# Optimization experiments

Hardware: AMD Instinct MI355X
Metric: run time of the kernel (lower is better)

The kernel has to match this reference:

```python
import math
import jax, jax.numpy as jnp
import numpy as np

B, T, C = 4, 2048, 1024
NH, HD = 16, C // 16
FF = 4096
EPS = 1e-5


def _layernorm(x, g, b):
    mu = jnp.mean(x, axis=-1, keepdims=True)
    var = jnp.mean(jnp.square(x - mu), axis=-1, keepdims=True)
    return (x - mu) * jax.lax.rsqrt(var + EPS) * g + b


def _new_gelu(x):
    c = math.sqrt(2.0 / math.pi)
    return 0.5 * x * (1.0 + jnp.tanh(c * (x + 0.044715 * x * x * x)))


def setup_inputs() -> dict:
    key = jax.random.key(0)
    ks = jax.random.split(key, 5)
    s = lambda fan_in: 1.0 / math.sqrt(fan_in)
    return {
        "x": jax.random.normal(ks[0], (B, T, C), jnp.float32),
        "ln1_g": jnp.ones((C,), jnp.float32),
        "ln1_b": jnp.zeros((C,), jnp.float32),
        "w_qkv": jax.random.normal(ks[1], (C, 3 * C), jnp.float32) * s(C),
        "b_qkv": jnp.zeros((3 * C,), jnp.float32),
        "w_attn_proj": jax.random.normal(ks[2], (C, C), jnp.float32) * s(C),
        "b_attn_proj": jnp.zeros((C,), jnp.float32),
        "ln2_g": jnp.ones((C,), jnp.float32),
        "ln2_b": jnp.zeros((C,), jnp.float32),
        "w_fc": jax.random.normal(ks[3], (C, FF), jnp.float32) * s(C),
        "b_fc": jnp.zeros((FF,), jnp.float32),
        "w_mlp_proj": jax.random.normal(ks[4], (FF, C), jnp.float32) * s(FF),
        "b_mlp_proj": jnp.zeros((C,), jnp.float32),
    }


def reference(x, ln1_g, ln1_b, w_qkv, b_qkv, w_attn_proj, b_attn_proj,
              ln2_g, ln2_b, w_fc, b_fc, w_mlp_proj, b_mlp_proj):
    # --- attention branch ---
    h = _layernorm(x, ln1_g, ln1_b)
    qkv = h @ w_qkv + b_qkv                      # [B,T,3C]
    q, k, v = jnp.split(qkv, 3, axis=-1)
    # [B,T,C] -> [B,NH,T,HD]
    to_heads = lambda t: t.reshape(B, T, NH, HD).transpose(0, 2, 1, 3)
    q, k, v = to_heads(q), to_heads(k), to_heads(v)
    scores = jnp.einsum("bhqd,bhkd->bhqk", q, k) / math.sqrt(HD)  # [B,NH,T,T]
    causal = jnp.tril(jnp.ones((T, T), bool))
    scores = jnp.where(causal, scores, -jnp.inf)
    probs = jax.nn.softmax(scores, axis=-1)
    attn = jnp.einsum("bhqk,bhkd->bhqd", probs, v)  # [B,NH,T,HD]
    attn = attn.transpose(0, 2, 1, 3).reshape(B, T, C)
    x = x + attn @ w_attn_proj + b_attn_proj
    # --- MLP branch ---
    h = _layernorm(x, ln2_g, ln2_b)
    h = _new_gelu(h @ w_fc + b_fc)
    x = x + h @ w_mlp_proj + b_mlp_proj
    return x
```

## Files before the change

kernel.cpp:

```cpp
#include <hip/hip_runtime.h>
#include <hip/hip_bf16.h>

typedef __bf16 bf16x8 __attribute__((ext_vector_type(8)));
typedef __bf16 bf16x4 __attribute__((ext_vector_type(4)));
typedef float f32x4 __attribute__((ext_vector_type(4)));

#define BM 128
#define BN 128
#define BK 32

__device__ __forceinline__ void gload16(const __bf16* g, __bf16* l) {
    __builtin_amdgcn_global_load_lds((const __attribute__((address_space(1))) void*)g,
                                     (__attribute__((address_space(3))) void*)l, 16, 0, 0);
}

__device__ __forceinline__ float gelu_f(float v) {
    float z = 0.7978845608028654f * (v + 0.044715f * v * v * v);
    float e = __expf(2.f * z);
    return 0.5f * v * (2.f - 2.f / (e + 1.f));
}

__global__ __launch_bounds__(256) void diag_kernel(float* out, int n, float v) {
    int i = blockIdx.x * 256 + threadIdx.x;
    if (i < n) out[i] = v;
}

__global__ __launch_bounds__(256) void cvtT_kernel(
    const float* __restrict__ in, __bf16* __restrict__ out, int K, int N)
{
    __shared__ __bf16 tile[32][33];
    int bx = blockIdx.x * 32, by = blockIdx.y * 32;
    int tx = threadIdx.x & 31, ty = threadIdx.x >> 5;
#pragma unroll
    for (int i = 0; i < 32; i += 8)
        tile[ty + i][tx] = (__bf16)in[(size_t)(by + ty + i) * N + bx + tx];
    __syncthreads();
#pragma unroll
    for (int i = 0; i < 32; i += 8)
        out[(size_t)(bx + ty + i) * K + by + tx] = tile[tx][ty + i];
}

__global__ __launch_bounds__(256) void ln_kernel(
    const float* __restrict__ x, const float* __restrict__ g,
    const float* __restrict__ bta, __bf16* __restrict__ out,
    const float* __restrict__ bias2, float* __restrict__ out2)
{
    const int row = blockIdx.x, t = threadIdx.x;
    const float* xr = x + (size_t)row * 1024;
    float4 xv = ((const float4*)xr)[t];
    float f[4] = {xv.x, xv.y, xv.z, xv.w};
    float s = f[0] + f[1] + f[2] + f[3];
    float ss = f[0]*f[0] + f[1]*f[1] + f[2]*f[2] + f[3]*f[3];
#pragma unroll
    for (int off = 32; off; off >>= 1) {
        s  += __shfl_xor(s, off, 64);
        ss += __shfl_xor(ss, off, 64);
    }
    __shared__ float red[8];
    int lane = t & 63, w = t >> 6;
    if (lane == 0) { red[w] = s; red[4 + w] = ss; }
    __syncthreads();
    s  = red[0] + red[1] + red[2] + red[3];
    ss = red[4] + red[5] + red[6] + red[7];
    float mu = s * (1.f / 1024.f);
    float var = ss * (1.f / 1024.f) - mu * mu;
    float rstd = rsqrtf(fmaxf(var, 0.f) + 1e-5f);
    float4 gv = ((const float4*)g)[t];
    float4 bv = ((const float4*)bta)[t];
    bf16x4 ov;
    ov[0] = (__bf16)((f[0] - mu) * rstd * gv.x + bv.x);
    ov[1] = (__bf16)((f[1] - mu) * rstd * gv.y + bv.y);
    ov[2] = (__bf16)((f[2] - mu) * rstd * gv.z + bv.z);
    ov[3] = (__bf16)((f[3] - mu) * rstd * gv.w + bv.w);
    ((bf16x4*)(out + (size_t)row * 1024))[t] = ov;
    if (out2) {
        float4 b2 = ((const float4*)bias2)[t];
        float4 o2 = {f[0] + b2.x, f[1] + b2.y, f[2] + b2.z, f[3] + b2.w};
        ((float4*)(out2 + (size_t)row * 1024))[t] = o2;
    }
}

template <int EPI, bool OUT32, int NSPLIT>
__global__ __launch_bounds__(256, 4) void gemm_bt_kernel(
    const __bf16* __restrict__ A, const __bf16* __restrict__ BT,
    const float* __restrict__ bias, const float* __restrict__ res,
    void* __restrict__ Cp, int M, int N, int K, int lda, int ldb)
{
    __shared__ __align__(16) __bf16 lA[2][BM * BK];
    __shared__ __align__(16) __bf16 lB[2][BN * BK];
    const int t = threadIdx.x;
    const int lane = t & 63;
    const int wave = t >> 6;
    const int wm = wave >> 1, wn = wave & 1;
    const int q4 = lane >> 4, r16 = lane & 15;
    const int bm = blockIdx.y * BM, bn = blockIdx.x * BN;
    const int Klen = K / NSPLIT;
    const int koff = (NSPLIT > 1) ? (int)blockIdx.z * Klen : 0;

    const int srow = t & 127;
    const int skc = t >> 7;
    const __bf16* ga0 = A + (size_t)(bm + srow) * lda + koff + skc * 8;
    const __bf16* ga1 = ga0 + 16;
    const __bf16* gb0 = BT + (size_t)(bn + srow) * ldb + koff + skc * 8;
    const __bf16* gb1 = gb0 + 16;

    f32x4 acc[4][4];
    f32x4 zero4 = {0.f, 0.f, 0.f, 0.f};
#pragma unroll
    for (int mi = 0; mi < 4; ++mi)
#pragma unroll
        for (int ni = 0; ni < 4; ++ni) acc[mi][ni] = zero4;

    gload16(ga0, &lA[0][t * 8]);
    gload16(ga1, &lA[0][t * 8 + 2048]);
    gload16(gb0, &lB[0][t * 8]);
    gload16(gb1, &lB[0][t * 8 + 2048]);
    ga0 += BK; ga1 += BK; gb0 += BK; gb1 += BK;
    __syncthreads();

    const int nk = Klen / BK;
    int cur = 0;
    for (int it = 0; it < nk; ++it) {
        if (it + 1 < nk) {
            gload16(ga0, &lA[cur ^ 1][t * 8]);
            gload16(ga1, &lA[cur ^ 1][t * 8 + 2048]);
            gload16(gb0, &lB[cur ^ 1][t * 8]);
            gload16(gb1, &lB[cur ^ 1][t * 8 + 2048]);
            ga0 += BK; ga1 += BK; gb0 += BK; gb1 += BK;
        }
        bf16x8 af[4], bfr[4];
#pragma unroll
        for (int i = 0; i < 4; ++i)
            af[i] = *(const bf16x8*)&lA[cur][q4 * 1024 + (wm * 64 + i * 16 + r16) * 8];
#pragma unroll
        for (int i = 0; i < 4; ++i)
            bfr[i] = *(const bf16x8*)&lB[cur][q4 * 1024 + (wn * 64 + i * 16 + r16) * 8];
#pragma unroll
        for (int mi = 0; mi < 4; ++mi)
#pragma unroll
            for (int ni = 0; ni < 4; ++ni)
                acc[mi][ni] = __builtin_amdgcn_mfma_f32_16x16x32_bf16(
                    af[mi], bfr[ni], acc[mi][ni], 0, 0, 0);
        if (it + 1 < nk) __syncthreads();
        cur ^= 1;
    }

#pragma unroll
    for (int mi = 0; mi < 4; ++mi) {
#pragma unroll
        for (int ni = 0; ni < 4; ++ni) {
#pragma unroll
            for (int i = 0; i < 4; ++i) {
                int r = bm + wm * 64 + mi * 16 + q4 * 4 + i;
                int c = bn + wn * 64 + ni * 16 + r16;
                if (EPI == 3) {
                    atomicAdd((float*)Cp + (size_t)r * N + c, acc[mi][ni][i]);
                } else {
                    float v = acc[mi][ni][i] + bias[c];
                    if (EPI == 1) v += res[(size_t)r * N + c];
                    if (EPI == 2) v = gelu_f(v);
                    if (OUT32) ((float*)Cp)[(size_t)r * N + c] = v;
                    else       ((__bf16*)Cp)[(size_t)r * N + c] = (__bf16)v;
                }
            }
        }
    }
}

template <int EPI, bool OUT32>
__global__ __launch_bounds__(256, 2) void gemm_bt_wide_kernel(
    const __bf16* __restrict__ A, const __bf16* __restrict__ BT,
    const float* __restrict__ bias, const float* __restrict__ res,
    void* __restrict__ Cp, int M, int N, int K)
{
    __shared__ __align__(16) __bf16 lA[2][128 * BK];
    __shared__ __align__(16) __bf16 lB[2][256 * BK];
    const int t = threadIdx.x;
    const int lane = t & 63;
    const int wave = t >> 6;
    const int wm = wave >> 1, wn = wave & 1;
    const int q4 = lane >> 4, r16 = lane & 15;
    const int bm = blockIdx.y * 128, bn = blockIdx.x * 256;

    const int srow = t & 127;
    const int skc = t >> 7;
    const __bf16* ga0 = A + (size_t)(bm + srow) * K + skc * 8;
    const __bf16* ga1 = ga0 + 16;
    const __bf16* gb  = BT + (size_t)(bn + t) * K;

    f32x4 acc[4][8];
    f32x4 zero4 = {0.f, 0.f, 0.f, 0.f};
#pragma unroll
    for (int mi = 0; mi < 4; ++mi)
#pragma unroll
        for (int ni = 0; ni < 8; ++ni) acc[mi][ni] = zero4;

    gload16(ga0, &lA[0][t * 8]);
    gload16(ga1, &lA[0][t * 8 + 2048]);
#pragma unroll
    for (int c = 0; c < 4; ++c)
        gload16(gb + c * 8, &lB[0][c * 2048 + t * 8]);
    ga0 += BK; ga1 += BK; gb += BK;
    __syncthreads();

    const int nk = K / BK;
    int cur = 0;
    for (int it = 0; it < nk; ++it) {
        if (it + 1 < nk) {
            gload16(ga0, &lA[cur ^ 1][t * 8]);
            gload16(ga1, &lA[cur ^ 1][t * 8 + 2048]);
#pragma unroll
            for (int c = 0; c < 4; ++c)
                gload16(gb + c * 8, &lB[cur ^ 1][c * 2048 + t * 8]);
            ga0 += BK; ga1 += BK; gb += BK;
        }
        bf16x8 af[4], bfr[8];
#pragma unroll
        for (int i = 0; i < 4; ++i)
            af[i] = *(const bf16x8*)&lA[cur][q4 * 1024 + (wm * 64 + i * 16 + r16) * 8];
#pragma unroll
        for (int i = 0; i < 8; ++i)
            bfr[i] = *(const bf16x8*)&lB[cur][q4 * 2048 + (wn * 128 + i * 16 + r16) * 8];
#pragma unroll
        for (int mi = 0; mi < 4; ++mi)
#pragma unroll
            for (int ni = 0; ni < 8; ++ni)
                acc[mi][ni] = __builtin_amdgcn_mfma_f32_16x16x32_bf16(
                    af[mi], bfr[ni], acc[mi][ni], 0, 0, 0);
        if (it + 1 < nk) __syncthreads();
        cur ^= 1;
    }

#pragma unroll
    for (int mi = 0; mi < 4; ++mi) {
#pragma unroll
        for (int ni = 0; ni < 8; ++ni) {
#pragma unroll
            for (int i = 0; i < 4; ++i) {
                int r = bm + wm * 64 + mi * 16 + q4 * 4 + i;
                int c = bn + wn * 128 + ni * 16 + r16;
                float v = acc[mi][ni][i] + bias[c];
                if (EPI == 1) v += res[(size_t)r * N + c];
                if (EPI == 2) v = gelu_f(v);
                if (OUT32) ((float*)Cp)[(size_t)r * N + c] = v;
                else       ((__bf16*)Cp)[(size_t)r * N + c] = (__bf16)v;
            }
        }
    }
}

__global__ __launch_bounds__(256, 4) void attn_kernel(
    const __bf16* __restrict__ qkv, __bf16* __restrict__ attnb)
{
    __shared__ __align__(16) __bf16 lK[8192];
    __shared__ __align__(16) __bf16 lV[8192];
    __shared__ __align__(16) __bf16 lP[4][512];

    const int t = threadIdx.x, lane = t & 63, w = t >> 6;
    const int q4 = lane >> 4, r16 = lane & 15;
    const int b = blockIdx.y >> 4, h = blockIdx.y & 15;
    const int qt = (blockIdx.x + (blockIdx.y >> 4) * 4) & 15;
    const int qb = qt * 128;
    const __bf16* Qb = qkv + (size_t)b * 2048 * 3072 + h * 64;
    const __bf16* Kb = Qb + 1024;
    const __bf16* Vb = Qb + 2048;

    bf16x8 qf[2][2];
#pragma unroll
    for (int p = 0; p < 2; ++p) {
        int qrow = qb + p * 64 + w * 16 + r16;
        qf[p][0] = *(const bf16x8*)(Qb + (size_t)qrow * 3072 + q4 * 8);
        qf[p][1] = *(const bf16x8*)(Qb + (size_t)qrow * 3072 + 32 + q4 * 8);
#pragma unroll
        for (int j = 0; j < 8; ++j) {
            qf[p][0][j] = (__bf16)((float)qf[p][0][j] * 0.125f);
            qf[p][1][j] = (__bf16)((float)qf[p][1][j] * 0.125f);
        }
    }

    f32x4 zero4 = {0.f, 0.f, 0.f, 0.f};
    f32x4 o[2][4];
    float rs[2][4];
#pragma unroll
    for (int p = 0; p < 2; ++p)
#pragma unroll
        for (int i = 0; i < 4; ++i) { o[p][i] = zero4; rs[p][i] = 0.f; }

    const int skey = t & 127;
    const int vkc = t >> 6, svd = t & 63;

    for (int kb = 0; kb < qb + 128; kb += 128) {
        __syncthreads();
#pragma unroll
        for (int c = 0; c < 4; ++c)
            gload16(Kb + (size_t)(kb + skey) * 3072 + (c * 2 + (t >> 7)) * 8,
                    &lK[c * 2048 + t * 8]);
#pragma unroll
        for (int c = 0; c < 4; ++c) {
            int kc = c * 4 + vkc;
            bf16x8 vt;
#pragma unroll
            for (int j = 0; j < 8; ++j)
                vt[j] = Vb[(size_t)(kb + kc * 8 + j) * 3072 + svd];
            *(bf16x8*)&lV[kc * 512 + svd * 8] = vt;
        }
        __syncthreads();

#pragma unroll
        for (int p = 0; p < 2; ++p) {
            const int row0 = qb + p * 64 + w * 16 + q4 * 4;
            const bool interior = (kb + 127) <= (qb + p * 64 + w * 16);

            f32x4 s[8];
#pragma unroll
            for (int kg = 0; kg < 8; ++kg) {
                bf16x8 kfA = *(const bf16x8*)&lK[q4 * 1024 + (kg * 16 + r16) * 8];
                bf16x8 kfB = *(const bf16x8*)&lK[(4 + q4) * 1024 + (kg * 16 + r16) * 8];
                s[kg] = __builtin_amdgcn_mfma_f32_16x16x32_bf16(qf[p][0], kfA, zero4, 0, 0, 0);
                s[kg] = __builtin_amdgcn_mfma_f32_16x16x32_bf16(qf[p][1], kfB, s[kg], 0, 0, 0);
            }

#pragma unroll
            for (int kg = 0; kg < 8; ++kg)
#pragma unroll
                for (int i = 0; i < 4; ++i) {
                    float e = __expf(fminf(s[kg][i], 75.f));
                    if (!interior && (kb + kg * 16 + r16) > (row0 + i)) e = 0.f;
                    s[kg][i] = e;
                    rs[p][i] += e;
                }

#pragma unroll
            for (int c = 0; c < 4; ++c) {
#pragma unroll
                for (int kh = 0; kh < 2; ++kh)
#pragma unroll
                    for (int i = 0; i < 4; ++i)
                        lP[w][(kh * 2 + (r16 >> 3)) * 128 + (q4 * 4 + i) * 8 + (r16 & 7)] =
                            (__bf16)s[c * 2 + kh][i];
                asm volatile("s_waitcnt lgkmcnt(0)" ::: "memory");
                bf16x8 pf = *(const bf16x8*)&lP[w][q4 * 128 + r16 * 8];
#pragma unroll
                for (int ci = 0; ci < 4; ++ci) {
                    bf16x8 vf = *(const bf16x8*)&lV[(c * 4 + q4) * 512 + (ci * 16 + r16) * 8];
                    o[p][ci] = __builtin_amdgcn_mfma_f32_16x16x32_bf16(pf, vf, o[p][ci], 0, 0, 0);
                }
            }
        }
    }

#pragma unroll
    for (int p = 0; p < 2; ++p) {
#pragma unroll
        for (int off = 8; off; off >>= 1)
#pragma unroll
            for (int i = 0; i < 4; ++i) rs[p][i] += __shfl_xor(rs[p][i], off, 64);
#pragma unroll
        for (int ci = 0; ci < 4; ++ci)
#pragma unroll
            for (int i = 0; i < 4; ++i) {
                int trow = qb + p * 64 + w * 16 + q4 * 4 + i;
                float inv_l = (rs[p][i] > 0.f) ? (1.f / rs[p][i]) : 0.f;
                attnb[(size_t)(b * 2048 + trow) * 1024 + h * 64 + ci * 16 + r16] =
                    (__bf16)(o[p][ci][i] * inv_l);
            }
    }
}

extern "C" void kernel_launch(void* const* d_in, const int* in_sizes, int n_in,
                              void* d_out, int out_size, void* d_ws, size_t ws_size,
                              hipStream_t stream)
{
    const float* x      = (const float*)d_in[0];
    const float* ln1_g  = (const float*)d_in[1];
    const float* ln1_b  = (const float*)d_in[2];
    const float* w_qkv  = (const float*)d_in[3];
    const float* b_qkv  = (const float*)d_in[4];
    const float* w_proj = (const float*)d_in[5];
    const float* b_proj = (const float*)d_in[6];
    const float* ln2_g  = (const float*)d_in[7];
    const float* ln2_b  = (const float*)d_in[8];
    const float* w_fc   = (const float*)d_in[9];
    const float* b_fc   = (const float*)d_in[10];
    const float* w_mlp  = (const float*)d_in[11];
    const float* b_mlp  = (const float*)d_in[12];
    float* out = (float*)d_out;

    const size_t MiB = (size_t)1 << 20;
    if (ws_size < 136 * MiB) {
        float v = 1000.f + (float)(ws_size >> 20);
        diag_kernel<<<(out_size + 255) / 256, 256, 0, stream>>>(out, out_size, v);
        return;
    }

    char* ws = (char*)d_ws;
    __bf16* bufA   = (__bf16*)(ws);
    __bf16* bufB   = (__bf16*)(ws + 16 * MiB);
    float*  x1     = (float*) (ws + 80 * MiB);
    __bf16* wqkvT  = (__bf16*)(ws + 112 * MiB);
    __bf16* wprojT = (__bf16*)(ws + 118 * MiB);
    __bf16* wfcT   = (__bf16*)(ws + 120 * MiB);
    __bf16* wmlpT  = (__bf16*)(ws + 128 * MiB);

    cvtT_kernel<<<dim3(96, 32),  256, 0, stream>>>(w_qkv,  wqkvT,  1024, 3072);
    cvtT_kernel<<<dim3(32, 32),  256, 0, stream>>>(w_proj, wprojT, 1024, 1024);
    cvtT_kernel<<<dim3(128, 32), 256, 0, stream>>>(w_fc,   wfcT,   1024, 4096);
    cvtT_kernel<<<dim3(32, 128), 256, 0, stream>>>(w_mlp,  wmlpT,  4096, 1024);

    ln_kernel<<<8192, 256, 0, stream>>>(x, ln1_g, ln1_b, bufA, nullptr, nullptr);
    gemm_bt_wide_kernel<0, false><<<dim3(12, 64), 256, 0, stream>>>(
        bufA, wqkvT, b_qkv, nullptr, bufB, 8192, 3072, 1024);
    attn_kernel<<<dim3(16, 64), 256, 0, stream>>>(bufB, bufA);
    gemm_bt_kernel<1, true, 1><<<dim3(8, 64), 256, 0, stream>>>(
        bufA, wprojT, b_proj, x, x1, 8192, 1024, 1024, 1024, 1024);
    ln_kernel<<<8192, 256, 0, stream>>>(x1, ln2_g, ln2_b, bufA, b_mlp, out);
    gemm_bt_wide_kernel<2, false><<<dim3(16, 64), 256, 0, stream>>>(
        bufA, wfcT, b_fc, nullptr, bufB, 8192, 4096, 1024);
    gemm_bt_kernel<3, true, 2><<<dim3(8, 64, 2), 256, 0, stream>>>(
        bufB, wmlpT, b_mlp, nullptr, out, 8192, 1024, 4096, 4096, 4096);
}
```

Measured before the change: 743.0 us.

## Remap workgroups across XCDs and replace split-K atomics with fused residual epilogue

Adds an XCD-aware swizzle of the flat workgroup index in both GEMM kernels and the attention kernel, so that tiles sharing A or B panels land on the same XCD and can reuse its L2. The final MLP projection no longer uses split-K with atomicAdd into a pre-initialised output. It now runs as a single-pass GEMM whose epilogue adds the bias and the x1 residual, which also removes the extra output write from the second layernorm. The trade-off is half as many workgroups for the K=4096 GEMM (512 instead of 1024), with a longer K loop each, in exchange for dropping the atomics and the extra memory traffic.

```diff
diff --git a/kernel.cpp b/kernel.cpp
--- a/kernel.cpp
+++ b/kernel.cpp
@@ -20,6 +20,10 @@
     return 0.5f * v * (2.f - 2.f / (e + 1.f));
 }
 
+__device__ __forceinline__ int xcd_swizzle(int flat, int nwg) {
+    return (flat & 7) * (nwg >> 3) + (flat >> 3);
+}
+
 __global__ __launch_bounds__(256) void diag_kernel(float* out, int n, float v) {
     int i = blockIdx.x * 256 + threadIdx.x;
     if (i < n) out[i] = v;
@@ -42,8 +46,7 @@
 
 __global__ __launch_bounds__(256) void ln_kernel(
     const float* __restrict__ x, const float* __restrict__ g,
-    const float* __restrict__ bta, __bf16* __restrict__ out,
-    const float* __restrict__ bias2, float* __restrict__ out2)
+    const float* __restrict__ bta, __bf16* __restrict__ out)
 {
     const int row = blockIdx.x, t = threadIdx.x;
     const float* xr = x + (size_t)row * 1024;
@@ -73,18 +76,13 @@
     ov[2] = (__bf16)((f[2] - mu) * rstd * gv.z + bv.z);
     ov[3] = (__bf16)((f[3] - mu) * rstd * gv.w + bv.w);
     ((bf16x4*)(out + (size_t)row * 1024))[t] = ov;
-    if (out2) {
-        float4 b2 = ((const float4*)bias2)[t];
-        float4 o2 = {f[0] + b2.x, f[1] + b2.y, f[2] + b2.z, f[3] + b2.w};
-        ((float4*)(out2 + (size_t)row * 1024))[t] = o2;
-    }
-}
-
-template <int EPI, bool OUT32, int NSPLIT>
+}
+
+template <int EPI, bool OUT32>
 __global__ __launch_bounds__(256, 4) void gemm_bt_kernel(
     const __bf16* __restrict__ A, const __bf16* __restrict__ BT,
     const float* __restrict__ bias, const float* __restrict__ res,
-    void* __restrict__ Cp, int M, int N, int K, int lda, int ldb)
+    void* __restrict__ Cp, int M, int N, int K)
 {
     __shared__ __align__(16) __bf16 lA[2][BM * BK];
     __shared__ __align__(16) __bf16 lB[2][BN * BK];
@@ -93,15 +91,15 @@
     const int wave = t >> 6;
     const int wm = wave >> 1, wn = wave & 1;
     const int q4 = lane >> 4, r16 = lane & 15;
-    const int bm = blockIdx.y * BM, bn = blockIdx.x * BN;
-    const int Klen = K / NSPLIT;
-    const int koff = (NSPLIT > 1) ? (int)blockIdx.z * Klen : 0;
+    const int nwg = gridDim.x * gridDim.y;
+    const int nf = xcd_swizzle(blockIdx.y * gridDim.x + blockIdx.x, nwg);
+    const int bm = (nf / gridDim.x) * BM, bn = (nf % gridDim.x) * BN;
 
     const int srow = t & 127;
     const int skc = t >> 7;
-    const __bf16* ga0 = A + (size_t)(bm + srow) * lda + koff + skc * 8;
+    const __bf16* ga0 = A + (size_t)(bm + srow) * K + skc * 8;
     const __bf16* ga1 = ga0 + 16;
-    const __bf16* gb0 = BT + (size_t)(bn + srow) * ldb + koff + skc * 8;
+    const __bf16* gb0 = BT + (size_t)(bn + srow) * K + skc * 8;
     const __bf16* gb1 = gb0 + 16;
 
     f32x4 acc[4][4];
@@ -118,7 +116,7 @@
     ga0 += BK; ga1 += BK; gb0 += BK; gb1 += BK;
     __syncthreads();
 
-    const int nk = Klen / BK;
+    const int nk = K / BK;
     int cur = 0;
     for (int it = 0; it < nk; ++it) {
         if (it + 1 < nk) {
@@ -153,15 +151,11 @@
             for (int i = 0; i < 4; ++i) {
                 int r = bm + wm * 64 + mi * 16 + q4 * 4 + i;
                 int c = bn + wn * 64 + ni * 16 + r16;
-                if (EPI == 3) {
-                    atomicAdd((float*)Cp + (size_t)r * N + c, acc[mi][ni][i]);
-                } else {
-                    float v = acc[mi][ni][i] + bias[c];
-                    if (EPI == 1) v += res[(size_t)r * N + c];
-                    if (EPI == 2) v = gelu_f(v);
-                    if (OUT32) ((float*)Cp)[(size_t)r * N + c] = v;
-                    else       ((__bf16*)Cp)[(size_t)r * N + c] = (__bf16)v;
-                }
+                float v = acc[mi][ni][i] + bias[c];
+                if (EPI == 1) v += res[(size_t)r * N + c];
+                if (EPI == 2) v = gelu_f(v);
+                if (OUT32) ((float*)Cp)[(size_t)r * N + c] = v;
+                else       ((__bf16*)Cp)[(size_t)r * N + c] = (__bf16)v;
             }
         }
     }
@@ -180,7 +174,9 @@
     const int wave = t >> 6;
     const int wm = wave >> 1, wn = wave & 1;
     const int q4 = lane >> 4, r16 = lane & 15;
-    const int bm = blockIdx.y * 128, bn = blockIdx.x * 256;
+    const int nwg = gridDim.x * gridDim.y;
+    const int nf = xcd_swizzle(blockIdx.y * gridDim.x + blockIdx.x, nwg);
+    const int bm = (nf / gridDim.x) * 128, bn = (nf % gridDim.x) * 256;
 
     const int srow = t & 127;
     const int skc = t >> 7;
@@ -258,8 +254,10 @@
 
     const int t = threadIdx.x, lane = t & 63, w = t >> 6;
     const int q4 = lane >> 4, r16 = lane & 15;
-    const int b = blockIdx.y >> 4, h = blockIdx.y & 15;
-    const int qt = (blockIdx.x + (blockIdx.y >> 4) * 4) & 15;
+    const int nf = xcd_swizzle(blockIdx.y * 16 + blockIdx.x, 1024);
+    const int qt = nf & 15;
+    const int bh = nf >> 4;
+    const int b = bh >> 4, h = bh & 15;
     const int qb = qt * 128;
     const __bf16* Qb = qkv + (size_t)b * 2048 * 3072 + h * 64;
     const __bf16* Kb = Qb + 1024;
@@ -407,15 +405,15 @@
     cvtT_kernel<<<dim3(128, 32), 256, 0, stream>>>(w_fc,   wfcT,   1024, 4096);
     cvtT_kernel<<<dim3(32, 128), 256, 0, stream>>>(w_mlp,  wmlpT,  4096, 1024);
 
-    ln_kernel<<<8192, 256, 0, stream>>>(x, ln1_g, ln1_b, bufA, nullptr, nullptr);
+    ln_kernel<<<8192, 256, 0, stream>>>(x, ln1_g, ln1_b, bufA);
     gemm_bt_wide_kernel<0, false><<<dim3(12, 64), 256, 0, stream>>>(
         bufA, wqkvT, b_qkv, nullptr, bufB, 8192, 3072, 1024);
     attn_kernel<<<dim3(16, 64), 256, 0, stream>>>(bufB, bufA);
-    gemm_bt_kernel<1, true, 1><<<dim3(8, 64), 256, 0, stream>>>(
-        bufA, wprojT, b_proj, x, x1, 8192, 1024, 1024, 1024, 1024);
-    ln_kernel<<<8192, 256, 0, stream>>>(x1, ln2_g, ln2_b, bufA, b_mlp, out);
+    gemm_bt_kernel<1, true><<<dim3(8, 64), 256, 0, stream>>>(
+        bufA, wprojT, b_proj, x, x1, 8192, 1024, 1024);
+    ln_kernel<<<8192, 256, 0, stream>>>(x1, ln2_g, ln2_b, bufA);
     gemm_bt_wide_kernel<2, false><<<dim3(16, 64), 256, 0, stream>>>(
         bufA, wfcT, b_fc, nullptr, bufB, 8192, 4096, 1024);
-    gemm_bt_kernel<3, true, 2><<<dim3(8, 64, 2), 256, 0, stream>>>(
-        bufB, wmlpT, b_mlp, nullptr, out, 8192, 1024, 4096, 4096, 4096);
-}
+    gemm_bt_kernel<1, true><<<dim3(8, 64), 256, 0, stream>>>(
+        bufB, wmlpT, b_mlp, x1, out, 8192, 1024, 4096);
+}
```

Result: faster. 702.9 us (-5.4%).
